# Optimization experiments

Hardware: AMD Instinct MI355X
Metric: run time of the kernel (lower is better)

The kernel has to match this reference:

```python
import jax, jax.numpy as jnp
import numpy as np

B, T = 64, 64
HUMAN, IN = 64, 8
HS, ES, K = 1024, 1024, 7
PSI_H, PSI_LR = 1024, 30

_PAR_SHAPES = [(HS, HS), (HS,), (IN, HS), (HS, HUMAN), (IN, HUMAN - IN)]
_PAR_SIZES = [int(np.prod(s)) for s in _PAR_SHAPES]
N_PSI = int(sum(_PAR_SIZES))
_OFFS = np.cumsum([0] + _PAR_SIZES)


def setup_inputs() -> dict:
    key = jax.random.key(0)
    ks = jax.random.split(key, 16)
    def xav(k, shape):
        lim = float(np.sqrt(6.0 / (shape[0] + shape[1])))
        return jax.random.uniform(k, shape, minval=-lim, maxval=lim, dtype=jnp.float32)
    def uni(k, shape, s):
        return jax.random.uniform(k, shape, minval=-s, maxval=s, dtype=jnp.float32)
    se = float(1.0 / np.sqrt(ES))
    return {
        "inputs": jax.random.normal(ks[0], (B, T, IN), jnp.float32),
        "outputs": jax.random.normal(ks[1], (B, T, HUMAN), jnp.float32),
        "eps": jax.random.normal(ks[2], (B, K), jnp.float32),
        "enc_Wih": uni(ks[3], (3 * ES, HUMAN), se),
        "enc_Whh": uni(ks[4], (3 * ES, ES), se),
        "enc_bih": uni(ks[5], (3 * ES,), se),
        "enc_bhh": uni(ks[6], (3 * ES,), se),
        "to_mu": xav(ks[7], (ES, K)),
        "to_lsigma": xav(ks[8], (ES, K)),
        "to_lsigma_bias": -0.5 * jnp.ones((K,), jnp.float32),
        "W1": xav(ks[9], (K, PSI_H)),
        "b1": jnp.zeros((PSI_H,), jnp.float32),
        "W2": xav(ks[10], (PSI_H, PSI_LR)),
        "b2": jnp.zeros((PSI_LR,), jnp.float32),
        "W3": xav(ks[11], (PSI_LR, N_PSI)),
        "b3": jnp.zeros((N_PSI,), jnp.float32),
        "gru_Wih": xav(ks[12], (IN, 2 * HS)),
        "gru_Whh": xav(ks[13], (HS, 2 * HS)),
        "gru_bias": jnp.concatenate([jnp.zeros((HS,)), jnp.ones((HS,))]).astype(jnp.float32),
    }


def _gru_cell(h, x, Wih, Whh, bih, bhh):
    # torch.nn.GRUCell math, gate order (r, z, n)
    gx = x @ Wih.T + bih
    gh = h @ Whh.T + bhh
    xr, xz, xn = jnp.split(gx, 3, axis=-1)
    hr, hz, hn = jnp.split(gh, 3, axis=-1)
    r = jax.nn.sigmoid(xr + hr)
    z = jax.nn.sigmoid(xz + hz)
    n = jnp.tanh(xn + r * hn)
    return (1.0 - z) * n + z * h


def _split_psi(psi):
    # psi: [B, N_PSI] -> per-sample (Whh, bh, Wih, C, D)
    return [psi[:, _OFFS[i]:_OFFS[i + 1]].reshape((-1,) + _PAR_SHAPES[i]) for i in range(5)]


def reference(inputs, outputs, eps, enc_Wih, enc_Whh, enc_bih, enc_bhh,
              to_mu, to_lsigma, to_lsigma_bias, W1, b1, W2, b2, W3, b3,
              gru_Wih, gru_Whh, gru_bias):
    bsz = inputs.shape[0]
    # ---- encoder: GRUCell over time-major outputs ----
    out_tm = jnp.swapaxes(outputs, 0, 1)  # [T, B, HUMAN]
    h0 = jnp.zeros((bsz, ES), inputs.dtype)
    h_enc = _gru_cell(h0, out_tm[0], enc_Wih, enc_Whh, enc_bih, enc_bhh)
    def enc_step(h, x):
        h = _gru_cell(h, x, enc_Wih, enc_Whh, enc_bih, enc_bhh)
        return h, None
    h_enc, _ = jax.lax.scan(enc_step, h_enc, out_tm[1:])
    mu = h_enc @ to_mu                       # [B, K]
    logstd = h_enc @ to_lsigma + to_lsigma_bias
    z = mu + eps * jnp.exp(logstd)
    # ---- hypernetwork psi decoder ----
    psi = (jnp.tanh(z @ W1 + b1) @ W2 + b2) @ W3 + b3   # [B, N_PSI]
    Whh_b, bh_b, Wih_b, C_b, D_b = _split_psi(psi)
    # ---- per-sample GRU decoder, vectorized over batch, scan over time ----
    gx_all = jnp.einsum('bti,ij->tbj', inputs, gru_Wih)  # [T, B, 2*HS]
    xW_all = jnp.einsum('bti,bih->tbh', inputs, Wih_b)   # [T, B, HS]

    def dec_step(h, xs):
        gx_t, xW_t = xs
        pre = gx_t + h @ gru_Whh + gru_bias   # [B, 2*HS]
        z_t = jax.nn.sigmoid(pre[:, :HS])
        r_t = jax.nn.sigmoid(pre[:, HS:])
        hWhh = jnp.einsum('bh,bhk->bk', h, Whh_b) + bh_b
        eta = jnp.tanh(xW_t + r_t * jnp.tanh(hWhh))
        h_new = z_t * h + (1.0 - z_t) * eta
        return h_new, h_new

    state0 = jnp.zeros((bsz, HS), inputs.dtype)
    h_last, dec_seq = jax.lax.scan(dec_step, state0, (gx_all, xW_all))
    dec_seq = jnp.swapaxes(dec_seq, 0, 1)    # [B, T, HS]
    # ---- readout ----
    yhats = jnp.einsum('bth,bhm->btm', dec_seq, C_b)
    xD = jnp.einsum('bti,bim->btm', inputs, D_b)  # [B, T, HUMAN-IN]
    yhats = yhats + jnp.concatenate([jnp.zeros_like(inputs), xD], axis=-1)
    # residual output
    yhats = yhats + jnp.concatenate(
        [inputs, jnp.zeros((bsz, inputs.shape[1], HUMAN - IN), inputs.dtype)], axis=-1)
    states = jax.lax.stop_gradient(h_last)
    return yhats, mu, logstd, states
```

## Files before the change

kernel.cpp:

```cpp
#include <hip/hip_runtime.h>

namespace {
constexpr int nT = 64;
constexpr int nK = 7;
constexpr long N_PSI = 1123776;
constexpr long SZ_WHH = 1048576;
constexpr long REST_SZ = 75200;
constexpr long R_BH = 0;
constexpr long R_WIH = 1024;
constexpr long R_C = 9216;
constexpr long R_D = 74752;
constexpr int NCH = 16;
constexpr long PHALF = (long)NCH * 64 * 1024;
}

typedef __attribute__((ext_vector_type(4))) unsigned short us4;

__device__ __forceinline__ float b2f(unsigned short u) {
  return __uint_as_float(((unsigned int)u) << 16);
}
__device__ __forceinline__ unsigned short f2b(float f) {
  unsigned int u = __float_as_uint(f);
  return (unsigned short)((u + 0x7fffu + ((u >> 16) & 1u)) >> 16);
}
__device__ __forceinline__ float sigm(float x) { return 1.f / (1.f + __expf(-x)); }

__global__ void transpose_bf16_k(const float* __restrict__ in, unsigned short* __restrict__ out,
                                 int rows, int cols) {
  __shared__ float tile[32][33];
  int x = blockIdx.x * 32 + threadIdx.x;
  int y = blockIdx.y * 32 + threadIdx.y;
  #pragma unroll
  for (int i = 0; i < 32; i += 8)
    if ((y + i) < rows && x < cols) tile[threadIdx.y + i][threadIdx.x] = in[(long)(y + i) * cols + x];
  __syncthreads();
  x = blockIdx.y * 32 + threadIdx.x;
  y = blockIdx.x * 32 + threadIdx.y;
  #pragma unroll
  for (int i = 0; i < 32; i += 8)
    if ((y + i) < cols && x < rows) out[(long)(y + i) * rows + x] = f2b(tile[threadIdx.x][threadIdx.y + i]);
}

__global__ void cvt_bf16_k(const float* __restrict__ in, unsigned short* __restrict__ out, long n) {
  long i = (long)blockIdx.x * 256 + threadIdx.x;
  if (i < n) out[i] = f2b(in[i]);
}

__global__ __launch_bounds__(256) void enc_gx_k(const float* __restrict__ outputs,
                                                const unsigned short* __restrict__ WtWihB,
                                                const float* __restrict__ bih,
                                                unsigned short* __restrict__ gxE) {
  int g0 = blockIdx.x * 256;
  int btg = blockIdx.y;
  __shared__ unsigned short ws[64 * 256];
  __shared__ float xs[64][64];
  for (int i = threadIdx.x; i < 64 * 256; i += 256)
    ws[i] = WtWihB[(long)(i >> 8) * 3072 + g0 + (i & 255)];
  for (int i = threadIdx.x; i < 64 * 64; i += 256) {
    int idx = btg * 64 + (i >> 6);
    int t = idx >> 6, b = idx & 63;
    xs[i >> 6][i & 63] = outputs[((long)b * nT + t) * 64 + (i & 63)];
  }
  __syncthreads();
  float bihv = bih[g0 + threadIdx.x];
  for (int j = 0; j < 64; ++j) {
    int idx = btg * 64 + j;
    float acc = bihv;
    #pragma unroll 8
    for (int i = 0; i < 64; ++i) acc += xs[j][i] * b2f(ws[i * 256 + threadIdx.x]);
    gxE[(long)idx * 3072 + g0 + threadIdx.x] = f2b(acc);
  }
}

__global__ __launch_bounds__(256) void dec_gx_k(const float* __restrict__ inputs,
                                                const float* __restrict__ gWih,
                                                const float* __restrict__ gbias,
                                                unsigned short* __restrict__ gxD) {
  int g0 = blockIdx.x * 256;
  int btg = blockIdx.y;
  __shared__ float ws[8][256];
  __shared__ float xs[64][8];
  for (int i = threadIdx.x; i < 8 * 256; i += 256)
    ws[i >> 8][i & 255] = gWih[(long)(i >> 8) * 2048 + g0 + (i & 255)];
  for (int i = threadIdx.x; i < 64 * 8; i += 256) {
    int idx = btg * 64 + (i >> 3);
    int t = idx >> 6, b = idx & 63;
    xs[i >> 3][i & 7] = inputs[((long)b * nT + t) * 8 + (i & 7)];
  }
  __syncthreads();
  float bv = gbias[g0 + threadIdx.x];
  for (int j = 0; j < 64; ++j) {
    int idx = btg * 64 + j;
    float acc = bv;
    #pragma unroll
    for (int i = 0; i < 8; ++i) acc += xs[j][i] * ws[i][threadIdx.x];
    gxD[(long)idx * 2048 + g0 + threadIdx.x] = f2b(acc);
  }
}

__global__ __launch_bounds__(256) void xW_k(const float* __restrict__ inputs,
                                            const float* __restrict__ Rest,
                                            unsigned short* __restrict__ xWb) {
  int k0 = blockIdx.x * 256;
  int b = blockIdx.y;
  __shared__ float ws[8][256];
  __shared__ float xs[64][8];
  const float* RB = Rest + (long)b * REST_SZ + R_WIH;
  for (int i = threadIdx.x; i < 8 * 256; i += 256)
    ws[i >> 8][i & 255] = RB[(long)(i >> 8) * 1024 + k0 + (i & 255)];
  for (int i = threadIdx.x; i < 64 * 8; i += 256)
    xs[i >> 3][i & 7] = inputs[((long)b * nT + (i >> 3)) * 8 + (i & 7)];
  __syncthreads();
  for (int t = 0; t < 64; ++t) {
    float acc = 0.f;
    #pragma unroll
    for (int i = 0; i < 8; ++i) acc += xs[t][i] * ws[i][threadIdx.x];
    xWb[((long)t * 64 + b) * 1024 + k0 + threadIdx.x] = f2b(acc);
  }
}

__global__ __launch_bounds__(512, 2) void enc_step3_k(
    const unsigned short* __restrict__ W,
    const unsigned short* __restrict__ gxE,
    const float* __restrict__ bhh,
    float* __restrict__ hEnc,
    const float* __restrict__ pRr, const float* __restrict__ pZr, const float* __restrict__ pNr,
    float* __restrict__ pRw, float* __restrict__ pZw, float* __restrict__ pNw,
    int t) {
  int c = blockIdx.x & (NCH - 1);
  int sp = blockIdx.x >> 4;
  int b0 = sp * 2, b1 = b0 + 1;
  __shared__ float h0s[64], h1s[64];
  __shared__ float red[3][4][128];
  int v = threadIdx.x;
  {
    int q = v >> 7, idx = v & 127;
    int bb = (idx >> 6) ? b1 : b0;
    int e = c * 64 + (idx & 63);
    float sr = 0.f, sz = 0.f, sn = 0.f;
    if (t > 0) {
      #pragma unroll
      for (int cc = q * 4; cc < q * 4 + 4; ++cc) {
        long base = ((long)cc * 64 + bb) * 1024 + e;
        sr += pRr[base]; sz += pZr[base]; sn += pNr[base];
      }
    }
    red[0][q][idx] = sr; red[1][q][idx] = sz; red[2][q][idx] = sn;
  }
  __syncthreads();
  if (v < 128) {
    int hi = v >> 6;
    int bb = hi ? b1 : b0;
    int e = c * 64 + (v & 63);
    float sr = red[0][0][v] + red[0][1][v] + red[0][2][v] + red[0][3][v];
    float sz = red[1][0][v] + red[1][1][v] + red[1][2][v] + red[1][3][v];
    float sn = red[2][0][v] + red[2][1][v] + red[2][2][v] + red[2][3][v];
    long gb = ((long)t * 64 + bb) * 3072;
    float xr = b2f(gxE[gb + e]), xz = b2f(gxE[gb + 1024 + e]), xn = b2f(gxE[gb + 2048 + e]);
    float hr = sr + bhh[e], hz = sz + bhh[1024 + e], hn = sn + bhh[2048 + e];
    float r = sigm(xr + hr);
    float z = sigm(xz + hz);
    float n = tanhf(xn + r * hn);
    float hold = (t > 0) ? hEnc[(long)bb * 1024 + e] : 0.f;
    float hnew = (1.f - z) * n + z * hold;
    hEnc[(long)bb * 1024 + e] = hnew;
    if (hi) h1s[v & 63] = hnew; else h0s[v & 63] = hnew;
  }
  __syncthreads();
  if (t < nT - 1) {
    if (v < 256) {
      int e0 = v * 4;
      float ar0[4] = {}, az0[4] = {}, ar1[4] = {}, az1[4] = {};
      const unsigned short* Wb = W + (long)(c * 64) * 3072 + e0;
      #pragma unroll 4
      for (int j = 0; j < 64; ++j) {
        us4 wr = *(const us4*)(Wb + (long)j * 3072);
        us4 wz = *(const us4*)(Wb + (long)j * 3072 + 1024);
        float hv0 = h0s[j], hv1 = h1s[j];
        #pragma unroll
        for (int q = 0; q < 4; ++q) {
          float fr = b2f(wr[q]), fz = b2f(wz[q]);
          ar0[q] += hv0 * fr; az0[q] += hv0 * fz;
          ar1[q] += hv1 * fr; az1[q] += hv1 * fz;
        }
      }
      long i0 = ((long)c * 64 + b0) * 1024 + e0;
      long i1 = i0 + 1024;
      *(float4*)(pRw + i0) = make_float4(ar0[0], ar0[1], ar0[2], ar0[3]);
      *(float4*)(pZw + i0) = make_float4(az0[0], az0[1], az0[2], az0[3]);
      *(float4*)(pRw + i1) = make_float4(ar1[0], ar1[1], ar1[2], ar1[3]);
      *(float4*)(pZw + i1) = make_float4(az1[0], az1[1], az1[2], az1[3]);
    } else {
      int e0 = (v - 256) * 4;
      float an0[4] = {}, an1[4] = {};
      const unsigned short* Wb = W + (long)(c * 64) * 3072 + 2048 + e0;
      #pragma unroll 8
      for (int j = 0; j < 64; ++j) {
        us4 wn = *(const us4*)(Wb + (long)j * 3072);
        float hv0 = h0s[j], hv1 = h1s[j];
        #pragma unroll
        for (int q = 0; q < 4; ++q) {
          float fn = b2f(wn[q]);
          an0[q] += hv0 * fn; an1[q] += hv1 * fn;
        }
      }
      long i0 = ((long)c * 64 + b0) * 1024 + e0;
      long i1 = i0 + 1024;
      *(float4*)(pNw + i0) = make_float4(an0[0], an0[1], an0[2], an0[3]);
      *(float4*)(pNw + i1) = make_float4(an1[0], an1[1], an1[2], an1[3]);
    }
  }
}

__global__ __launch_bounds__(256) void latent_hyper_k(
    const float* __restrict__ h_enc,
    const float* __restrict__ to_mu, const float* __restrict__ to_lsig,
    const float* __restrict__ lsig_bias, const float* __restrict__ eps,
    const float* __restrict__ W1, const float* __restrict__ b1,
    const float* __restrict__ W2, const float* __restrict__ b2,
    float* __restrict__ out_mu, float* __restrict__ out_lsig,
    float* __restrict__ a2out) {
  int b = blockIdx.x;
  __shared__ float hs[1024];
  __shared__ float zv[8];
  __shared__ float a1[1024];
  for (int i = threadIdx.x; i < 1024; i += 256) hs[i] = h_enc[b * 1024 + i];
  __syncthreads();
  int g = threadIdx.x >> 5, s = threadIdx.x & 31;
  if (g < nK) {
    float am = 0.f, as_ = 0.f;
    for (int h = s; h < 1024; h += 32) {
      float hv = hs[h];
      am += hv * to_mu[h * nK + g];
      as_ += hv * to_lsig[h * nK + g];
    }
    #pragma unroll
    for (int m = 16; m >= 1; m >>= 1) { am += __shfl_xor(am, m); as_ += __shfl_xor(as_, m); }
    if (s == 0) {
      float ls = as_ + lsig_bias[g];
      out_mu[b * nK + g] = am;
      out_lsig[b * nK + g] = ls;
      zv[g] = am + eps[b * nK + g] * __expf(ls);
    }
  }
  __syncthreads();
  for (int j = threadIdx.x; j < 1024; j += 256) {
    float acc = b1[j];
    #pragma unroll
    for (int i = 0; i < nK; ++i) acc += zv[i] * W1[i * 1024 + j];
    a1[j] = tanhf(acc);
  }
  __syncthreads();
  int l = threadIdx.x >> 3, s8 = threadIdx.x & 7;
  if (l < 30) {
    float acc = 0.f;
    for (int j = s8; j < 1024; j += 8) acc += a1[j] * W2[j * 30 + l];
    acc += __shfl_xor(acc, 4);
    acc += __shfl_xor(acc, 2);
    acc += __shfl_xor(acc, 1);
    if (s8 == 0) a2out[b * 30 + l] = acc + b2[l];
  }
}

__global__ __launch_bounds__(256) void psi_max_k(
    const float* __restrict__ a2, const float* __restrict__ W3, const float* __restrict__ b3,
    unsigned* __restrict__ pmax) {
  __shared__ float sa[64 * 30];
  __shared__ float wm[4][64];
  for (int i = threadIdx.x; i < 64 * 30; i += 256) sa[i] = a2[i];
  long n0 = (long)blockIdx.x * 256 + threadIdx.x;
  int h = (int)(n0 >> 10);
  __syncthreads();
  float acc[64];
  float bb = b3[n0];
  #pragma unroll
  for (int b = 0; b < 64; ++b) acc[b] = bb;
  for (int l = 0; l < 30; ++l) {
    float w = W3[(long)l * N_PSI + n0];
    #pragma unroll
    for (int b = 0; b < 64; ++b) acc[b] += sa[b * 30 + l] * w;
  }
  int lane = threadIdx.x & 63, wv = threadIdx.x >> 6;
  #pragma unroll
  for (int b = 0; b < 64; ++b) {
    float m = fabsf(acc[b]);
    #pragma unroll
    for (int d = 32; d >= 1; d >>= 1) m = fmaxf(m, __shfl_xor(m, d));
    if (lane == 0) wm[wv][b] = m;
  }
  __syncthreads();
  if (threadIdx.x < 64) {
    int b = threadIdx.x;
    float m = fmaxf(fmaxf(wm[0][b], wm[1][b]), fmaxf(wm[2][b], wm[3][b]));
    atomicMax(&pmax[b * 1024 + h], __float_as_uint(m));
  }
}

__global__ void wscale2_k(const unsigned* __restrict__ pmax,
                          float* __restrict__ sdec, float* __restrict__ sinv) {
  int i = blockIdx.x * 256 + threadIdx.x;
  float m = __uint_as_float(pmax[i]);
  sdec[i] = m / 127.f;
  sinv[i] = (m > 0.f) ? 127.f / m : 0.f;
}

__global__ __launch_bounds__(256) void psi_q_k(
    const float* __restrict__ a2, const float* __restrict__ W3, const float* __restrict__ b3,
    const float* __restrict__ sinv, char* __restrict__ Q8, float* __restrict__ Rest) {
  __shared__ float sa[64 * 30];
  for (int i = threadIdx.x; i < 64 * 30; i += 256) sa[i] = a2[i];
  long n0 = (long)blockIdx.x * 256 + threadIdx.x;
  __syncthreads();
  if (n0 >= N_PSI) return;
  float acc[64];
  float bb = b3[n0];
  #pragma unroll
  for (int b = 0; b < 64; ++b) acc[b] = bb;
  for (int l = 0; l < 30; ++l) {
    float w = W3[(long)l * N_PSI + n0];
    #pragma unroll
    for (int b = 0; b < 64; ++b) acc[b] += sa[b * 30 + l] * w;
  }
  if (n0 < SZ_WHH) {
    int h = (int)(n0 >> 10);
    const float* si = sinv + h;
    #pragma unroll
    for (int b = 0; b < 64; ++b) {
      int q = __float2int_rn(acc[b] * si[b * 1024]);
      q = min(127, max(-127, q));
      Q8[(long)b * SZ_WHH + n0] = (char)q;
    }
  } else {
    long r = n0 - SZ_WHH;
    #pragma unroll
    for (int b = 0; b < 64; ++b) Rest[(long)b * REST_SZ + r] = acc[b];
  }
}

__global__ __launch_bounds__(512, 2) void dec_step_q8d_k(
    const char* __restrict__ Q8,
    const float* __restrict__ sdec,
    const unsigned short* __restrict__ gWhhB,
    const unsigned short* __restrict__ gxD,
    const unsigned short* __restrict__ xWb,
    const float* __restrict__ Rest,
    float* __restrict__ decS,
    const float* __restrict__ pZr, const float* __restrict__ pRr, const float* __restrict__ pWr,
    float* __restrict__ pZw, float* __restrict__ pRw, float* __restrict__ pWw,
    int t) {
  int c = blockIdx.x & (NCH - 1);
  int sp = blockIdx.x >> 4;
  int b0 = sp * 2, b1 = b0 + 1;
  __shared__ float h0s[64], h1s[64];
  __shared__ float h0q[64], h1q[64];
  __shared__ float red[3][4][128];
  int v = threadIdx.x;
  {
    int q = v >> 7, idx = v & 127;
    int bb = (idx >> 6) ? b1 : b0;
    int k = c * 64 + (idx & 63);
    float sz = 0.f, sr = 0.f, sw = 0.f;
    if (t > 0) {
      #pragma unroll
      for (int cc = q * 4; cc < q * 4 + 4; ++cc) {
        long base = ((long)cc * 64 + bb) * 1024 + k;
        sz += pZr[base]; sr += pRr[base]; sw += pWr[base];
      }
    }
    red[0][q][idx] = sz; red[1][q][idx] = sr; red[2][q][idx] = sw;
  }
  __syncthreads();
  if (v < 128) {
    int hi = v >> 6;
    int bb = hi ? b1 : b0;
    int k = c * 64 + (v & 63);
    float sz = red[0][0][v] + red[0][1][v] + red[0][2][v] + red[0][3][v];
    float sr = red[1][0][v] + red[1][1][v] + red[1][2][v] + red[1][3][v];
    float sw = red[2][0][v] + red[2][1][v] + red[2][2][v] + red[2][3][v];
    long gb = ((long)t * 64 + bb) * 2048;
    float gz = b2f(gxD[gb + k]), gr = b2f(gxD[gb + 1024 + k]);
    float z = sigm(gz + sz);
    float r = sigm(gr + sr);
    float hW = sw + Rest[(long)bb * REST_SZ + R_BH + k];
    float xw = b2f(xWb[((long)t * 64 + bb) * 1024 + k]);
    float eta = tanhf(xw + r * tanhf(hW));
    float hold = (t > 0) ? decS[((long)bb * nT + (t - 1)) * 1024 + k] : 0.f;
    float hnew = z * hold + (1.f - z) * eta;
    decS[((long)bb * nT + t) * 1024 + k] = hnew;
    float hsc = hnew * sdec[(long)bb * 1024 + k];
    if (hi) { h1s[v & 63] = hnew; h1q[v & 63] = hsc; }
    else    { h0s[v & 63] = hnew; h0q[v & 63] = hsc; }
  }
  __syncthreads();
  if (t < nT - 1) {
    if (v < 256) {
      int k0 = v * 4;
      float az0[4] = {}, ar0[4] = {}, az1[4] = {}, ar1[4] = {};
      const unsigned short* G = gWhhB + (long)(c * 64) * 2048 + k0;
      #pragma unroll 4
      for (int j = 0; j < 64; ++j) {
        us4 wz = *(const us4*)(G + (long)j * 2048);
        us4 wr = *(const us4*)(G + (long)j * 2048 + 1024);
        float hv0 = h0s[j], hv1 = h1s[j];
        #pragma unroll
        for (int q = 0; q < 4; ++q) {
          float fz = b2f(wz[q]), fr = b2f(wr[q]);
          az0[q] += hv0 * fz; ar0[q] += hv0 * fr;
          az1[q] += hv1 * fz; ar1[q] += hv1 * fr;
        }
      }
      long i0 = ((long)c * 64 + b0) * 1024 + k0;
      long i1 = i0 + 1024;
      *(float4*)(pZw + i0) = make_float4(az0[0], az0[1], az0[2], az0[3]);
      *(float4*)(pRw + i0) = make_float4(ar0[0], ar0[1], ar0[2], ar0[3]);
      *(float4*)(pZw + i1) = make_float4(az1[0], az1[1], az1[2], az1[3]);
      *(float4*)(pRw + i1) = make_float4(ar1[0], ar1[1], ar1[2], ar1[3]);
    } else {
      int k0 = (v - 256) * 4;
      float aw0[4] = {}, aw1[4] = {};
      const char* Q0 = Q8 + (long)b0 * SZ_WHH + (long)(c * 64) * 1024 + k0;
      const char* Q1 = Q8 + (long)b1 * SZ_WHH + (long)(c * 64) * 1024 + k0;
      #pragma unroll 8
      for (int j = 0; j < 64; ++j) {
        char4 q0 = *(const char4*)(Q0 + (long)j * 1024);
        char4 q1 = *(const char4*)(Q1 + (long)j * 1024);
        float hv0 = h0q[j], hv1 = h1q[j];
        aw0[0] += hv0 * (float)q0.x; aw0[1] += hv0 * (float)q0.y;
        aw0[2] += hv0 * (float)q0.z; aw0[3] += hv0 * (float)q0.w;
        aw1[0] += hv1 * (float)q1.x; aw1[1] += hv1 * (float)q1.y;
        aw1[2] += hv1 * (float)q1.z; aw1[3] += hv1 * (float)q1.w;
      }
      long i0 = ((long)c * 64 + b0) * 1024 + k0;
      long i1 = i0 + 1024;
      *(float4*)(pWw + i0) = make_float4(aw0[0], aw0[1], aw0[2], aw0[3]);
      *(float4*)(pWw + i1) = make_float4(aw1[0], aw1[1], aw1[2], aw1[3]);
    }
  }
}

__global__ __launch_bounds__(256) void readout_k(
    const float* __restrict__ dec_seq, const float* __restrict__ inputs,
    const float* __restrict__ Rest, float* __restrict__ yhats) {
  int b = blockIdx.x >> 3;
  int tg = blockIdx.x & 7;
  __shared__ float ss[8][1024];
  __shared__ float part[4][8][64];
  for (int i = threadIdx.x; i < 8 * 1024; i += 256)
    ss[i >> 10][i & 1023] = dec_seq[((long)b * nT + tg * 8 + (i >> 10)) * 1024 + (i & 1023)];
  __syncthreads();
  int m = threadIdx.x & 63, hq = threadIdx.x >> 6;
  const float* C = Rest + (long)b * REST_SZ + R_C;
  float acc[8] = {};
  for (int h = hq * 256; h < hq * 256 + 256; ++h) {
    float cv = C[(long)h * 64 + m];
    #pragma unroll
    for (int tt = 0; tt < 8; ++tt) acc[tt] += ss[tt][h] * cv;
  }
  #pragma unroll
  for (int tt = 0; tt < 8; ++tt) part[hq][tt][m] = acc[tt];
  __syncthreads();
  const float* D = Rest + (long)b * REST_SZ + R_D;
  for (int o = threadIdx.x; o < 512; o += 256) {
    int tt = o >> 6, mm = o & 63;
    float a = part[0][tt][mm] + part[1][tt][mm] + part[2][tt][mm] + part[3][tt][mm];
    long bt = (long)b * nT + tg * 8 + tt;
    if (mm < 8) {
      a += inputs[bt * 8 + mm];
    } else {
      #pragma unroll
      for (int i = 0; i < 8; ++i) a += inputs[bt * 8 + i] * D[i * 56 + (mm - 8)];
    }
    yhats[bt * 64 + mm] = a;
  }
}

__global__ void copy_states_k(const float* __restrict__ dec_seq, float* __restrict__ states) {
  int i = blockIdx.x * 256 + threadIdx.x;
  int b = i >> 10, h = i & 1023;
  states[i] = dec_seq[((long)b * nT + (nT - 1)) * 1024 + h];
}

extern "C" void kernel_launch(void* const* d_in, const int* in_sizes, int n_in,
                              void* d_out, int out_size, void* d_ws, size_t ws_size,
                              hipStream_t stream) {
  const float* inputs  = (const float*)d_in[0];
  const float* outputs = (const float*)d_in[1];
  const float* eps     = (const float*)d_in[2];
  const float* enc_Wih = (const float*)d_in[3];
  const float* enc_Whh = (const float*)d_in[4];
  const float* enc_bih = (const float*)d_in[5];
  const float* enc_bhh = (const float*)d_in[6];
  const float* to_mu   = (const float*)d_in[7];
  const float* to_lsig = (const float*)d_in[8];
  const float* lsig_b  = (const float*)d_in[9];
  const float* W1 = (const float*)d_in[10];
  const float* b1 = (const float*)d_in[11];
  const float* W2 = (const float*)d_in[12];
  const float* b2 = (const float*)d_in[13];
  const float* W3 = (const float*)d_in[14];
  const float* b3 = (const float*)d_in[15];
  const float* gWih  = (const float*)d_in[16];
  const float* gWhh  = (const float*)d_in[17];
  const float* gbias = (const float*)d_in[18];

  char* ws = (char*)d_ws;
  size_t off = 0;
  auto alloc = [&](size_t bytes) { size_t o = off; off = (off + bytes + 255) & ~(size_t)255; return o; };
  size_t oRest   = alloc(64ull * REST_SZ * 4);
  size_t oQ8     = alloc(64ull * SZ_WHH);
  size_t ogWhhB  = alloc(1024ull * 2048 * 2);
  size_t oWtWhhB = alloc(1024ull * 3072 * 2);
  size_t oWtWihB = alloc(64ull * 3072 * 2);
  size_t ogxE    = alloc(64ull * 64 * 3072 * 2);
  size_t ogxD    = alloc(64ull * 64 * 2048 * 2);
  size_t oxWb    = alloc(64ull * 64 * 1024 * 2);
  size_t opA     = alloc((size_t)2 * PHALF * 4);
  size_t opB     = alloc((size_t)2 * PHALF * 4);
  size_t opC     = alloc((size_t)2 * PHALF * 4);
  size_t ohA     = alloc(64ull * 1024 * 4);
  size_t oDec    = alloc(64ull * 64 * 1024 * 4);
  size_t oA2     = alloc(64 * 30 * 4);
  size_t oPmax   = alloc(64ull * 1024 * 4);
  size_t oSdec   = alloc(64ull * 1024 * 4);
  size_t oSinv   = alloc(64ull * 1024 * 4);
  (void)in_sizes; (void)n_in; (void)out_size; (void)ws_size;

  float*          Rest   = (float*)(ws + oRest);
  char*           Q8     = (char*)(ws + oQ8);
  unsigned short* gWhhB  = (unsigned short*)(ws + ogWhhB);
  unsigned short* WtWhhB = (unsigned short*)(ws + oWtWhhB);
  unsigned short* WtWihB = (unsigned short*)(ws + oWtWihB);
  unsigned short* gxE    = (unsigned short*)(ws + ogxE);
  unsigned short* gxD    = (unsigned short*)(ws + ogxD);
  unsigned short* xWb    = (unsigned short*)(ws + oxWb);
  float* pA   = (float*)(ws + opA);
  float* pB   = (float*)(ws + opB);
  float* pC   = (float*)(ws + opC);
  float* hA   = (float*)(ws + ohA);
  float* decS = (float*)(ws + oDec);
  float* a2   = (float*)(ws + oA2);
  unsigned* pmax = (unsigned*)(ws + oPmax);
  float* sdec = (float*)(ws + oSdec);
  float* sinv = (float*)(ws + oSinv);

  float* out    = (float*)d_out;
  float* out_yh = out;
  float* out_mu = out + 262144;
  float* out_ls = out + 262144 + 448;
  float* out_st = out + 262144 + 896;

  hipMemsetAsync(pmax, 0, 64ull * 1024 * 4, stream);

  transpose_bf16_k<<<dim3(32, 96), dim3(32, 8), 0, stream>>>(enc_Whh, WtWhhB, 3072, 1024);
  transpose_bf16_k<<<dim3(2, 96),  dim3(32, 8), 0, stream>>>(enc_Wih, WtWihB, 3072, 64);
  cvt_bf16_k<<<(int)((1024ull * 2048 + 255) / 256), 256, 0, stream>>>(gWhh, gWhhB, 1024 * 2048);

  enc_gx_k<<<dim3(12, 64), 256, 0, stream>>>(outputs, WtWihB, enc_bih, gxE);

  for (int t = 0; t < nT; ++t) {
    int rp = t & 1, wp = (t + 1) & 1;
    enc_step3_k<<<512, 512, 0, stream>>>(WtWhhB, gxE, enc_bhh, hA,
        pA + (size_t)rp * PHALF, pB + (size_t)rp * PHALF, pC + (size_t)rp * PHALF,
        pA + (size_t)wp * PHALF, pB + (size_t)wp * PHALF, pC + (size_t)wp * PHALF, t);
  }

  latent_hyper_k<<<64, 256, 0, stream>>>(hA, to_mu, to_lsig, lsig_b, eps,
                                         W1, b1, W2, b2, out_mu, out_ls, a2);
  psi_max_k<<<(int)(SZ_WHH / 256), 256, 0, stream>>>(a2, W3, b3, pmax);
  wscale2_k<<<256, 256, 0, stream>>>(pmax, sdec, sinv);
  psi_q_k<<<(int)((N_PSI + 255) / 256), 256, 0, stream>>>(a2, W3, b3, sinv, Q8, Rest);

  dec_gx_k<<<dim3(8, 64), 256, 0, stream>>>(inputs, gWih, gbias, gxD);
  xW_k<<<dim3(4, 64), 256, 0, stream>>>(inputs, Rest, xWb);

  for (int t = 0; t < nT; ++t) {
    int rp = t & 1, wp = (t + 1) & 1;
    dec_step_q8d_k<<<512, 512, 0, stream>>>(Q8, sdec, gWhhB, gxD, xWb, Rest, decS,
        pA + (size_t)rp * PHALF, pB + (size_t)rp * PHALF, pC + (size_t)rp * PHALF,
        pA + (size_t)wp * PHALF, pB + (size_t)wp * PHALF, pC + (size_t)wp * PHALF, t);
  }

  readout_k<<<512, 256, 0, stream>>>(decS, inputs, Rest, out_yh);
  copy_states_k<<<256, 256, 0, stream>>>(decS, out_st);
}
```

Before: 2.995 ms.

## Fuse psi hypernet max and int8 quantization into one pass with half-row scales

The separate max-reduction, scale and quantize kernels that each recomputed the W3 projection are replaced by one kernel. Each block owns half a row of Whh and computes the per-sample absmax in-block, then quantizes immediately, which removes the atomics, the memset and the second full recompute of the psi matrix. The quantization scale becomes per half-row, so the decoder step now reads two scales and keeps two scaled hidden vectors. The Rest part moves to its own kernel, and both kernels use float2 vectorized loads with the weights kept in registers.

```diff
diff --git a/kernel.cpp b/kernel.cpp
--- a/kernel.cpp
+++ b/kernel.cpp
@@ -262,82 +262,79 @@
   }
 }
 
-__global__ __launch_bounds__(256) void psi_max_k(
+__global__ __launch_bounds__(256, 1) void psi_q8_k(
     const float* __restrict__ a2, const float* __restrict__ W3, const float* __restrict__ b3,
-    unsigned* __restrict__ pmax) {
+    char* __restrict__ Q8, float* __restrict__ sdec ) {
   __shared__ float sa[64 * 30];
-  __shared__ float wm[4][64];
+  __shared__ float wred[4][4];
   for (int i = threadIdx.x; i < 64 * 30; i += 256) sa[i] = a2[i];
-  long n0 = (long)blockIdx.x * 256 + threadIdx.x;
-  int h = (int)(n0 >> 10);
-  __syncthreads();
-  float acc[64];
-  float bb = b3[n0];
+  int h = blockIdx.x >> 1, half = blockIdx.x & 1;
+  long nbase = (long)h * 1024 + half * 512;
+  long n0 = nbase + threadIdx.x * 2;
+  float2 w[30];
   #pragma unroll
-  for (int b = 0; b < 64; ++b) acc[b] = bb;
-  for (int l = 0; l < 30; ++l) {
-    float w = W3[(long)l * N_PSI + n0];
-    #pragma unroll
-    for (int b = 0; b < 64; ++b) acc[b] += sa[b * 30 + l] * w;
-  }
+  for (int l = 0; l < 30; ++l) w[l] = *(const float2*)(W3 + (long)l * N_PSI + n0);
+  float2 bb = *(const float2*)(b3 + n0);
+  __syncthreads();
   int lane = threadIdx.x & 63, wv = threadIdx.x >> 6;
-  #pragma unroll
-  for (int b = 0; b < 64; ++b) {
-    float m = fabsf(acc[b]);
-    #pragma unroll
-    for (int d = 32; d >= 1; d >>= 1) m = fmaxf(m, __shfl_xor(m, d));
-    if (lane == 0) wm[wv][b] = m;
-  }
-  __syncthreads();
-  if (threadIdx.x < 64) {
-    int b = threadIdx.x;
-    float m = fmaxf(fmaxf(wm[0][b], wm[1][b]), fmaxf(wm[2][b], wm[3][b]));
-    atomicMax(&pmax[b * 1024 + h], __float_as_uint(m));
-  }
-}
-
-__global__ void wscale2_k(const unsigned* __restrict__ pmax,
-                          float* __restrict__ sdec, float* __restrict__ sinv) {
-  int i = blockIdx.x * 256 + threadIdx.x;
-  float m = __uint_as_float(pmax[i]);
-  sdec[i] = m / 127.f;
-  sinv[i] = (m > 0.f) ? 127.f / m : 0.f;
-}
-
-__global__ __launch_bounds__(256) void psi_q_k(
+  for (int bg = 0; bg < 16; ++bg) {
+    float v0[4], v1[4];
+    #pragma unroll
+    for (int s = 0; s < 4; ++s) {
+      int b = bg * 4 + s;
+      float a0 = bb.x, a1 = bb.y;
+      const float* ab = &sa[b * 30];
+      #pragma unroll
+      for (int l = 0; l < 30; ++l) { float av = ab[l]; a0 += av * w[l].x; a1 += av * w[l].y; }
+      v0[s] = a0; v1[s] = a1;
+    }
+    #pragma unroll
+    for (int s = 0; s < 4; ++s) {
+      float m = fmaxf(fabsf(v0[s]), fabsf(v1[s]));
+      #pragma unroll
+      for (int d = 32; d >= 1; d >>= 1) m = fmaxf(m, __shfl_xor(m, d));
+      if (lane == 0) wred[wv][s] = m;
+    }
+    __syncthreads();
+    #pragma unroll
+    for (int s = 0; s < 4; ++s) {
+      int b = bg * 4 + s;
+      float mm = fmaxf(fmaxf(wred[0][s], wred[1][s]), fmaxf(wred[2][s], wred[3][s]));
+      float inv = (mm > 0.f) ? 127.f / mm : 0.f;
+      int q0 = __float2int_rn(v0[s] * inv);
+      int q1 = __float2int_rn(v1[s] * inv);
+      q0 = min(127, max(-127, q0));
+      q1 = min(127, max(-127, q1));
+      *(char2*)(Q8 + (long)b * SZ_WHH + n0) = make_char2((char)q0, (char)q1);
+      if (threadIdx.x == 0) sdec[((long)b * 1024 + h) * 2 + half] = mm * (1.f / 127.f);
+    }
+    __syncthreads();
+  }
+}
+
+__global__ __launch_bounds__(256) void psi_rest_k(
     const float* __restrict__ a2, const float* __restrict__ W3, const float* __restrict__ b3,
-    const float* __restrict__ sinv, char* __restrict__ Q8, float* __restrict__ Rest) {
+    float* __restrict__ Rest) {
   __shared__ float sa[64 * 30];
   for (int i = threadIdx.x; i < 64 * 30; i += 256) sa[i] = a2[i];
-  long n0 = (long)blockIdx.x * 256 + threadIdx.x;
+  long n0 = SZ_WHH + ((long)blockIdx.x * 256 + threadIdx.x) * 2;
   __syncthreads();
   if (n0 >= N_PSI) return;
-  float acc[64];
-  float bb = b3[n0];
+  float2 w[30];
   #pragma unroll
-  for (int b = 0; b < 64; ++b) acc[b] = bb;
-  for (int l = 0; l < 30; ++l) {
-    float w = W3[(long)l * N_PSI + n0];
-    #pragma unroll
-    for (int b = 0; b < 64; ++b) acc[b] += sa[b * 30 + l] * w;
-  }
-  if (n0 < SZ_WHH) {
-    int h = (int)(n0 >> 10);
-    const float* si = sinv + h;
-    #pragma unroll
-    for (int b = 0; b < 64; ++b) {
-      int q = __float2int_rn(acc[b] * si[b * 1024]);
-      q = min(127, max(-127, q));
-      Q8[(long)b * SZ_WHH + n0] = (char)q;
-    }
-  } else {
-    long r = n0 - SZ_WHH;
-    #pragma unroll
-    for (int b = 0; b < 64; ++b) Rest[(long)b * REST_SZ + r] = acc[b];
-  }
-}
-
-__global__ __launch_bounds__(512, 2) void dec_step_q8d_k(
+  for (int l = 0; l < 30; ++l) w[l] = *(const float2*)(W3 + (long)l * N_PSI + n0);
+  float2 bb = *(const float2*)(b3 + n0);
+  long r = n0 - SZ_WHH;
+  for (int b = 0; b < 64; ++b) {
+    float a0 = bb.x, a1 = bb.y;
+    const float* ab = &sa[b * 30];
+    #pragma unroll
+    for (int l = 0; l < 30; ++l) { float av = ab[l]; a0 += av * w[l].x; a1 += av * w[l].y; }
+    *(float2*)(Rest + (long)b * REST_SZ + r) = make_float2(a0, a1);
+  }
+}
+
+__global__ __launch_bounds__(512, 2) void dec_step_q8f_k(
     const char* __restrict__ Q8,
     const float* __restrict__ sdec,
     const unsigned short* __restrict__ gWhhB,
@@ -352,7 +349,7 @@
   int sp = blockIdx.x >> 4;
   int b0 = sp * 2, b1 = b0 + 1;
   __shared__ float h0s[64], h1s[64];
-  __shared__ float h0q[64], h1q[64];
+  __shared__ float h0qA[64], h0qB[64], h1qA[64], h1qB[64];
   __shared__ float red[3][4][128];
   int v = threadIdx.x;
   {
@@ -387,9 +384,9 @@
     float hold = (t > 0) ? decS[((long)bb * nT + (t - 1)) * 1024 + k] : 0.f;
     float hnew = z * hold + (1.f - z) * eta;
     decS[((long)bb * nT + t) * 1024 + k] = hnew;
-    float hsc = hnew * sdec[(long)bb * 1024 + k];
-    if (hi) { h1s[v & 63] = hnew; h1q[v & 63] = hsc; }
-    else    { h0s[v & 63] = hnew; h0q[v & 63] = hsc; }
+    float2 sc = *(const float2*)(sdec + ((long)bb * 1024 + k) * 2);
+    if (hi) { h1s[v & 63] = hnew; h1qA[v & 63] = hnew * sc.x; h1qB[v & 63] = hnew * sc.y; }
+    else    { h0s[v & 63] = hnew; h0qA[v & 63] = hnew * sc.x; h0qB[v & 63] = hnew * sc.y; }
   }
   __syncthreads();
   if (t < nT - 1) {
@@ -417,6 +414,8 @@
       *(float4*)(pRw + i1) = make_float4(ar1[0], ar1[1], ar1[2], ar1[3]);
     } else {
       int k0 = (v - 256) * 4;
+      const float* hq0 = (k0 < 512) ? h0qA : h0qB;
+      const float* hq1 = (k0 < 512) ? h1qA : h1qB;
       float aw0[4] = {}, aw1[4] = {};
       const char* Q0 = Q8 + (long)b0 * SZ_WHH + (long)(c * 64) * 1024 + k0;
       const char* Q1 = Q8 + (long)b1 * SZ_WHH + (long)(c * 64) * 1024 + k0;
@@ -424,7 +423,7 @@
       for (int j = 0; j < 64; ++j) {
         char4 q0 = *(const char4*)(Q0 + (long)j * 1024);
         char4 q1 = *(const char4*)(Q1 + (long)j * 1024);
-        float hv0 = h0q[j], hv1 = h1q[j];
+        float hv0 = hq0[j], hv1 = hq1[j];
         aw0[0] += hv0 * (float)q0.x; aw0[1] += hv0 * (float)q0.y;
         aw0[2] += hv0 * (float)q0.z; aw0[3] += hv0 * (float)q0.w;
         aw1[0] += hv1 * (float)q1.x; aw1[1] += hv1 * (float)q1.y;
@@ -508,6 +507,7 @@
   auto alloc = [&](size_t bytes) { size_t o = off; off = (off + bytes + 255) & ~(size_t)255; return o; };
   size_t oRest   = alloc(64ull * REST_SZ * 4);
   size_t oQ8     = alloc(64ull * SZ_WHH);
+  size_t oSdec   = alloc(64ull * 1024 * 2 * 4);
   size_t ogWhhB  = alloc(1024ull * 2048 * 2);
   size_t oWtWhhB = alloc(1024ull * 3072 * 2);
   size_t oWtWihB = alloc(64ull * 3072 * 2);
@@ -520,13 +520,11 @@
   size_t ohA     = alloc(64ull * 1024 * 4);
   size_t oDec    = alloc(64ull * 64 * 1024 * 4);
   size_t oA2     = alloc(64 * 30 * 4);
-  size_t oPmax   = alloc(64ull * 1024 * 4);
-  size_t oSdec   = alloc(64ull * 1024 * 4);
-  size_t oSinv   = alloc(64ull * 1024 * 4);
   (void)in_sizes; (void)n_in; (void)out_size; (void)ws_size;
 
   float*          Rest   = (float*)(ws + oRest);
   char*           Q8     = (char*)(ws + oQ8);
+  float*          sdec   = (float*)(ws + oSdec);
   unsigned short* gWhhB  = (unsigned short*)(ws + ogWhhB);
   unsigned short* WtWhhB = (unsigned short*)(ws + oWtWhhB);
   unsigned short* WtWihB = (unsigned short*)(ws + oWtWihB);
@@ -539,9 +537,6 @@
   float* hA   = (float*)(ws + ohA);
   float* decS = (float*)(ws + oDec);
   float* a2   = (float*)(ws + oA2);
-  unsigned* pmax = (unsigned*)(ws + oPmax);
-  float* sdec = (float*)(ws + oSdec);
-  float* sinv = (float*)(ws + oSinv);
 
   float* out    = (float*)d_out;
   float* out_yh = out;
@@ -549,8 +544,6 @@
   float* out_ls = out + 262144 + 448;
   float* out_st = out + 262144 + 896;
 
-  hipMemsetAsync(pmax, 0, 64ull * 1024 * 4, stream);
-
   transpose_bf16_k<<<dim3(32, 96), dim3(32, 8), 0, stream>>>(enc_Whh, WtWhhB, 3072, 1024);
   transpose_bf16_k<<<dim3(2, 96),  dim3(32, 8), 0, stream>>>(enc_Wih, WtWihB, 3072, 64);
   cvt_bf16_k<<<(int)((1024ull * 2048 + 255) / 256), 256, 0, stream>>>(gWhh, gWhhB, 1024 * 2048);
@@ -566,16 +559,15 @@
 
   latent_hyper_k<<<64, 256, 0, stream>>>(hA, to_mu, to_lsig, lsig_b, eps,
                                          W1, b1, W2, b2, out_mu, out_ls, a2);
-  psi_max_k<<<(int)(SZ_WHH / 256), 256, 0, stream>>>(a2, W3, b3, pmax);
-  wscale2_k<<<256, 256, 0, stream>>>(pmax, sdec, sinv);
-  psi_q_k<<<(int)((N_PSI + 255) / 256), 256, 0, stream>>>(a2, W3, b3, sinv, Q8, Rest);
+  psi_q8_k<<<2048, 256, 0, stream>>>(a2, W3, b3, Q8, sdec);
+  psi_rest_k<<<(int)((REST_SZ / 2 + 255) / 256), 256, 0, stream>>>(a2, W3, b3, Rest);
 
   dec_gx_k<<<dim3(8, 64), 256, 0, stream>>>(inputs, gWih, gbias, gxD);
   xW_k<<<dim3(4, 64), 256, 0, stream>>>(inputs, Rest, xWb);
 
   for (int t = 0; t < nT; ++t) {
     int rp = t & 1, wp = (t + 1) & 1;
-    dec_step_q8d_k<<<512, 512, 0, stream>>>(Q8, sdec, gWhhB, gxD, xWb, Rest, decS,
+    dec_step_q8f_k<<<512, 512, 0, stream>>>(Q8, sdec, gWhhB, gxD, xWb, Rest, decS,
         pA + (size_t)rp * PHALF, pB + (size_t)rp * PHALF, pC + (size_t)rp * PHALF,
         pA + (size_t)wp * PHALF, pB + (size_t)wp * PHALF, pC + (size_t)wp * PHALF, t);
   }
```

Measured after the change: 2.768 ms. 7.6% less time.
